# Kernel tuning notes

Hardware: AMD Instinct MI355X
Metric: run time of the kernel (lower is better)

## Reference

```python
import jax, jax.numpy as jnp
import numpy as np

DN = ('NCHW', 'OIHW', 'NCHW')
B, C, H, W = 4, 64, 256, 256
MIP = 8          # max(8, C // 32)
RED = C // 16    # CBAM reduced channels
PS = 8           # FSAS patch size


def conv2d(x, w, padding=0, groups=1):
    return jax.lax.conv_general_dilated(
        x, w, (1, 1), [(padding, padding), (padding, padding)],
        dimension_numbers=DN, feature_group_count=groups)


def bn_eval(x, g, b, eps=1e-5):
    # BatchNorm with init running stats (mean=0, var=1), eval mode
    return x / jnp.sqrt(1.0 + eps) * g[None, :, None, None] + b[None, :, None, None]


def h_swish(x):
    return x * jnp.clip(x + 3.0, 0.0, 6.0) / 6.0


def setup_inputs() -> dict:
    key = jax.random.key(0)
    ks = jax.random.split(key, 12)
    s = 0.05
    d = {
        'x': jax.random.normal(ks[0], (B, C, H, W), jnp.float32),
        # CoordAttention
        'ca_conv1_w': jax.random.normal(ks[1], (MIP, C, 1, 1), jnp.float32) * s,
        'ca_conv1_b': jnp.zeros((MIP,), jnp.float32),
        'ca_bn_g': jnp.ones((MIP,), jnp.float32),
        'ca_bn_b': jnp.zeros((MIP,), jnp.float32),
        'ca_convh_w': jax.random.normal(ks[2], (C, MIP, 1, 1), jnp.float32) * s,
        'ca_convh_b': jnp.zeros((C,), jnp.float32),
        'ca_convw_w': jax.random.normal(ks[3], (C, MIP, 1, 1), jnp.float32) * s,
        'ca_convw_b': jnp.zeros((C,), jnp.float32),
        # FSAS (bias=False)
        'fsas_hidden_w': jax.random.normal(ks[4], (6 * C, C, 1, 1), jnp.float32) * s,
        'fsas_dw_w': jax.random.normal(ks[5], (6 * C, 1, 3, 3), jnp.float32) * s,
        'fsas_proj_w': jax.random.normal(ks[6], (C, 2 * C, 1, 1), jnp.float32) * s,
        'ln_w': jnp.ones((2 * C,), jnp.float32),
        'ln_b': jnp.zeros((2 * C,), jnp.float32),
        # Fusion
        'fus_conv1_w': jax.random.normal(ks[7], (2 * C, 2 * C, 3, 3), jnp.float32) * s,
        'fus_bn1_g': jnp.ones((2 * C,), jnp.float32),
        'fus_bn1_b': jnp.zeros((2 * C,), jnp.float32),
        'fus_conv2_w': jax.random.normal(ks[8], (C, 2 * C, 1, 1), jnp.float32) * s,
        'fus_bn2_g': jnp.ones((C,), jnp.float32),
        'fus_bn2_b': jnp.zeros((C,), jnp.float32),
        # CBAM
        'cbam_mlp1_w': jax.random.normal(ks[9], (RED, C, 1, 1), jnp.float32) * s,
        'cbam_mlp2_w': jax.random.normal(ks[10], (C, RED, 1, 1), jnp.float32) * s,
        'cbam_sa_w': jax.random.normal(ks[11], (1, 2, 7, 7), jnp.float32) * s,
        'residual_scale': jnp.float32(0.1),
    }
    return d


def _forward(x, ca_conv1_w, ca_conv1_b, ca_bn_g, ca_bn_b, ca_convh_w, ca_convh_b,
             ca_convw_w, ca_convw_b, fsas_hidden_w, fsas_dw_w, fsas_proj_w, ln_w, ln_b,
             fus_conv1_w, fus_bn1_g, fus_bn1_b, fus_conv2_w, fus_bn2_g, fus_bn2_b,
             cbam_mlp1_w, cbam_mlp2_w, cbam_sa_w, residual_scale):
    b, c, h, w = x.shape
    c2 = 2 * c

    # ---- CoordAttention branch ----
    xh = jnp.mean(x, axis=3, keepdims=True)                       # [B,C,H,1]
    xw = jnp.mean(x, axis=2, keepdims=True).transpose(0, 1, 3, 2)  # [B,C,W,1]
    y = jnp.concatenate([xh, xw], axis=2)                          # [B,C,H+W,1]
    y = conv2d(y, ca_conv1_w) + ca_conv1_b[None, :, None, None]
    y = h_swish(bn_eval(y, ca_bn_g, ca_bn_b))
    yh, yw = y[:, :, :h], y[:, :, h:]
    yw = yw.transpose(0, 1, 3, 2)
    a_h = jax.nn.sigmoid(conv2d(yh, ca_convh_w) + ca_convh_b[None, :, None, None])
    a_w = jax.nn.sigmoid(conv2d(yw, ca_convw_w) + ca_convw_b[None, :, None, None])
    ca_out = x * a_h * a_w

    # ---- FSAS branch ----
    hid = conv2d(x, fsas_hidden_w)                                 # [B,6C,H,W]
    hid = conv2d(hid, fsas_dw_w, padding=1, groups=6 * c)          # depthwise 3x3
    q, k, v = jnp.split(hid, 3, axis=1)                            # each [B,2C,H,W]

    def patch(t):  # [B,2C,H,W] -> [B,2C,H/8,W/8,8,8]
        return t.reshape(b, c2, h // PS, PS, w // PS, PS).transpose(0, 1, 2, 4, 3, 5)

    qf = jnp.fft.rfft2(patch(q))
    kf = jnp.fft.rfft2(patch(k))
    o = jnp.fft.irfft2(qf * kf, s=(PS, PS))
    o = o.transpose(0, 1, 2, 4, 3, 5).reshape(b, c2, h, w)

    # WithBias LayerNorm over channel dim (per pixel)
    mu = jnp.mean(o, axis=1, keepdims=True)
    var = jnp.var(o, axis=1, keepdims=True)
    on = (o - mu) / jnp.sqrt(var + 1e-5) * ln_w[None, :, None, None] + ln_b[None, :, None, None]
    fsas_out = conv2d(v * on, fsas_proj_w)                         # [B,C,H,W]

    # ---- Fusion ----
    f = conv2d(jnp.concatenate([ca_out, fsas_out], axis=1), fus_conv1_w, padding=1)
    f = jax.nn.gelu(bn_eval(f, fus_bn1_g, fus_bn1_b), approximate=False)
    f = bn_eval(conv2d(f, fus_conv2_w), fus_bn2_g, fus_bn2_b)

    z = x + residual_scale * f

    # ---- CBAM ----
    avg = jnp.mean(z, axis=(2, 3), keepdims=True)
    mx = jnp.max(z, axis=(2, 3), keepdims=True)

    def mlp(t):
        return conv2d(jax.nn.relu(conv2d(t, cbam_mlp1_w)), cbam_mlp2_w)

    z = z * jax.nn.sigmoid(mlp(avg) + mlp(mx))
    sa = jnp.concatenate([jnp.mean(z, axis=1, keepdims=True),
                          jnp.max(z, axis=1, keepdims=True)], axis=1)
    z = z * jax.nn.sigmoid(conv2d(sa, cbam_sa_w, padding=3))
    return jax.nn.gelu(z, approximate=False)


def reference(x, ca_conv1_w, ca_conv1_b, ca_bn_g, ca_bn_b, ca_convh_w, ca_convh_b,
              ca_convw_w, ca_convw_b, fsas_hidden_w, fsas_dw_w, fsas_proj_w, ln_w, ln_b,
              fus_conv1_w, fus_bn1_g, fus_bn1_b, fus_conv2_w, fus_bn2_g, fus_bn2_b,
              cbam_mlp1_w, cbam_mlp2_w, cbam_sa_w, residual_scale):
    return _forward(x, ca_conv1_w, ca_conv1_b, ca_bn_g, ca_bn_b, ca_convh_w, ca_convh_b,
                    ca_convw_w, ca_convw_b, fsas_hidden_w, fsas_dw_w, fsas_proj_w, ln_w, ln_b,
                    fus_conv1_w, fus_bn1_g, fus_bn1_b, fus_conv2_w, fus_bn2_g, fus_bn2_b,
                    cbam_mlp1_w, cbam_mlp2_w, cbam_sa_w, residual_scale)
```

## Files before the change

kernel.cpp:

```cpp
#include <hip/hip_runtime.h>
#include <math.h>

#define B_ 4
#define C_ 64
#define C2_ 128
#define C6_ 384
#define H_ 256
#define Wd_ 256
#define HW_ 65536
#define MIP_ 8
#define BNINV 0.9999950000374994f

typedef short bf16x8 __attribute__((ext_vector_type(8)));
typedef float f32x4 __attribute__((ext_vector_type(4)));
typedef unsigned short u16x8 __attribute__((ext_vector_type(8)));
typedef unsigned short u16x4 __attribute__((ext_vector_type(4)));
typedef unsigned int   u32x4 __attribute__((ext_vector_type(4)));

__device__ __forceinline__ float sigm(float x){ return 1.f/(1.f+expf(-x)); }
__device__ __forceinline__ float gelu_f(float x){ return 0.5f*x*(1.f+erff(x*0.7071067811865476f)); }
__device__ __forceinline__ unsigned short bfrnd(float f){
  unsigned u = __float_as_uint(f);
  unsigned r = u + 0x7FFFu + ((u>>16)&1u);
  return (unsigned short)(r>>16);
}
__device__ __forceinline__ float bf2f(unsigned short s){
  return __uint_as_float(((unsigned)s)<<16);
}

__global__ void k_rowmean(const float* __restrict__ x, float* __restrict__ xh){
  int row = blockIdx.x*4 + (threadIdx.x>>6);
  int lane = threadIdx.x & 63;
  const float* p = x + (size_t)row*Wd_;
  float s = p[lane]+p[lane+64]+p[lane+128]+p[lane+192];
  #pragma unroll
  for(int off=32; off>0; off>>=1) s += __shfl_down(s, off, 64);
  if(lane==0) xh[row] = s*(1.f/Wd_);
}

__global__ void k_colmean(const float* __restrict__ x, float* __restrict__ xw){
  int idx = blockIdx.x*256 + threadIdx.x;
  int w = idx & 255; int bc = idx >> 8;
  const float* p = x + (size_t)bc*HW_ + w;
  float s = 0.f;
  for(int h=0;h<H_;h++) s += p[h*Wd_];
  xw[idx] = s*(1.f/H_);
}

__global__ void k_ca_t(const float* __restrict__ xh, const float* __restrict__ xw,
                       const float* __restrict__ w1, const float* __restrict__ b1,
                       const float* __restrict__ bng, const float* __restrict__ bnb,
                       float* __restrict__ t){
  int idx = blockIdx.x*256 + threadIdx.x;
  int p = idx & 511; int m = (idx>>9)&7; int b = idx>>12;
  float acc = b1[m];
  #pragma unroll 8
  for(int c=0;c<C_;c++){
    float yv = (p<256) ? xh[(b*C_+c)*256 + p] : xw[(b*C_+c)*256 + (p-256)];
    acc += w1[m*C_+c]*yv;
  }
  float v = acc*BNINV*bng[m] + bnb[m];
  t[idx] = v * fminf(fmaxf(v+3.f,0.f),6.f)*(1.f/6.f);
}

__global__ void k_ca_a(const float* __restrict__ t,
                       const float* __restrict__ wh, const float* __restrict__ bh,
                       const float* __restrict__ ww, const float* __restrict__ bw,
                       float* __restrict__ ah, float* __restrict__ aw){
  int idx = blockIdx.x*256 + threadIdx.x;
  int p = idx & 511; int co = (idx>>9)&63; int b = idx>>15;
  bool isH = (p<256);
  const float* wm = isH ? wh : ww;
  float acc = isH ? bh[co] : bw[co];
  #pragma unroll
  for(int m=0;m<MIP_;m++) acc += wm[co*MIP_+m]*t[(b*MIP_+m)*512+p];
  float s = sigm(acc);
  if(isH) ah[(b*C_+co)*256+p] = s; else aw[(b*C_+co)*256+(p-256)] = s;
}

__global__ void __launch_bounds__(256) k_xprep(const float* __restrict__ x, unsigned short* __restrict__ xb){
  __shared__ float sm[64][65];
  int tid = threadIdx.x;
  int img = blockIdx.x >> 10;
  int p0 = (blockIdx.x & 1023)*64;
  int lane = tid & 63, wq = tid >> 6;
  #pragma unroll
  for(int cc=0; cc<16; ++cc){
    int c = cc*4 + wq;
    sm[c][lane] = x[(size_t)(img*C_+c)*HW_ + p0 + lane];
  }
  __syncthreads();
  int pl = tid >> 2;
  int c0 = (tid & 3) * 16;
  u16x8 lo, hi;
  #pragma unroll
  for(int i=0;i<8;i++)  lo[i] = bfrnd(sm[c0+i][pl]);
  #pragma unroll
  for(int i=0;i<8;i++)  hi[i] = bfrnd(sm[c0+8+i][pl]);
  unsigned short* dst = xb + ((size_t)img*HW_ + p0 + pl)*64 + c0;
  *(u16x8*)(dst)     = lo;
  *(u16x8*)(dst + 8) = hi;
}

__global__ void k_wprep(const float* __restrict__ w, unsigned short* __restrict__ wbt){
  int t = blockIdx.x*256 + threadIdx.x;
  const float* src = w + (size_t)t*9;
  int oc = t >> 7, ic = t & 127;
  #pragma unroll
  for(int tap=0; tap<9; ++tap)
    wbt[(size_t)(tap*128+oc)*128 + ic] = bfrnd(src[tap]);
}

__global__ void k_wprep2(const float* __restrict__ pw, const float* __restrict__ w2,
                         const float* __restrict__ hw, unsigned short* __restrict__ pwb,
                         unsigned short* __restrict__ w2b, unsigned short* __restrict__ wb1){
  int t = blockIdx.x*256 + threadIdx.x;
  if(t < 8192){ pwb[t] = bfrnd(pw[t]); w2b[t] = bfrnd(w2[t]); }
  wb1[t] = bfrnd(hw[t]);
}

__global__ void __launch_bounds__(256) k_hid0_mfma(const unsigned short* __restrict__ xb,
                                                   const unsigned short* __restrict__ wb1,
                                                   unsigned short* __restrict__ hid0b){
  int tid = threadIdx.x;
  int lane = tid & 63, wid = tid >> 6;
  int l15 = lane & 15, lk = lane >> 4;
  int p0 = blockIdx.x*128 + wid*32;
  int oc0 = blockIdx.y*96;
  f32x4 acc[6][2];
  #pragma unroll
  for(int m=0;m<6;m++)
    #pragma unroll
    for(int n=0;n<2;n++) acc[m][n] = (f32x4)0.f;
  #pragma unroll
  for(int kk=0; kk<2; ++kk){
    bf16x8 bfr[2];
    #pragma unroll
    for(int n=0;n<2;n++)
      bfr[n] = *(const bf16x8*)(xb + (size_t)(p0 + n*16 + l15)*64 + kk*32 + lk*8);
    #pragma unroll
    for(int m=0;m<6;m++){
      bf16x8 af = *(const bf16x8*)(wb1 + (size_t)(oc0 + m*16 + l15)*64 + kk*32 + lk*8);
      #pragma unroll
      for(int n=0;n<2;n++)
        acc[m][n] = __builtin_amdgcn_mfma_f32_16x16x32_bf16(af, bfr[n], acc[m][n], 0,0,0);
    }
  }
  #pragma unroll
  for(int n=0;n<2;n++){
    int p = p0 + n*16 + l15;
    #pragma unroll
    for(int m=0;m<6;m++){
      u16x4 v;
      #pragma unroll
      for(int r=0;r<4;r++) v[r] = bfrnd(acc[m][n][r]);
      *(u16x4*)(hid0b + (size_t)p*384 + oc0 + m*16 + lk*4) = v;
    }
  }
}

__global__ void __launch_bounds__(256) k_dw_bf(const unsigned short* __restrict__ hid0b,
                                               const float* __restrict__ wd,
                                               unsigned short* __restrict__ hidb){
  int tid = threadIdx.x;
  int cg = tid & 15;
  int tg = tid >> 4;
  int p0 = blockIdx.x*64;
  int h  = p0 >> 8;
  int w0 = (p0 & 255) + tg*4;
  int chb = blockIdx.y*128 + cg*8;

  float wreg[72];
  {
    const f32x4* wsrc = (const f32x4*)(wd + (size_t)chb*9);
    #pragma unroll
    for(int i=0;i<18;i++){
      f32x4 v = wsrc[i];
      wreg[4*i+0]=v[0]; wreg[4*i+1]=v[1]; wreg[4*i+2]=v[2]; wreg[4*i+3]=v[3];
    }
  }
  float acc[4][8];
  #pragma unroll
  for(int px=0;px<4;px++)
    #pragma unroll
    for(int e=0;e<8;e++) acc[px][e] = 0.f;

  #pragma unroll
  for(int ky=0; ky<3; ++ky){
    int hh = h + ky - 1;
    if((unsigned)hh >= 256u) continue;
    float row[6][8];
    #pragma unroll
    for(int c6=0; c6<6; ++c6){
      int ww = w0 + c6 - 1;
      u16x8 v8 = {0,0,0,0,0,0,0,0};
      if((unsigned)ww < 256u)
        v8 = *(const u16x8*)(hid0b + (size_t)(hh*256+ww)*384 + chb);
      #pragma unroll
      for(int e=0;e<8;e++) row[c6][e] = bf2f(v8[e]);
    }
    #pragma unroll
    for(int kx=0; kx<3; ++kx){
      #pragma unroll
      for(int px=0; px<4; ++px){
        #pragma unroll
        for(int e=0;e<8;e++)
          acc[px][e] += row[px+kx][e] * wreg[e*9 + ky*3 + kx];
      }
    }
  }
  #pragma unroll
  for(int px=0; px<4; ++px){
    u16x8 o8;
    #pragma unroll
    for(int e=0;e<8;e++) o8[e] = bfrnd(acc[px][e]);
    *(u16x8*)(hidb + (size_t)(p0 + tg*4 + px)*384 + chb) = o8;
  }
}

__global__ void __launch_bounds__(256) k_circ_bf(const unsigned short* __restrict__ hidb,
                                                 unsigned short* __restrict__ ob){
  __shared__ __align__(16) unsigned short lq[2][64][128];
  __shared__ __align__(16) unsigned short lkk[2][64][128];
  int tid = threadIdx.x;
  #pragma unroll
  for(int it=0; it<8; ++it){
    int s = it*256 + tid;
    int which = s >> 10, rem = s & 1023;
    int pix = rem >> 4, cg = rem & 15;
    int gp = blockIdx.x*2 + which;
    int ph = gp >> 5, pw = gp & 31;
    size_t pg = (size_t)((ph*8 + (pix>>3))*256 + pw*8 + (pix&7));
    *(u16x8*)&lq[which][pix][cg*8]  = *(const u16x8*)(hidb + pg*384 + cg*8);
    *(u16x8*)&lkk[which][pix][cg*8] = *(const u16x8*)(hidb + pg*384 + 128 + cg*8);
  }
  __syncthreads();
  int which = tid >> 7, c = tid & 127;
  float kr[64];
  #pragma unroll
  for(int pix=0;pix<64;pix++) kr[pix] = bf2f(lkk[which][pix][c]);
  float outv[64];
  #pragma unroll
  for(int t2=0;t2<64;t2++) outv[t2] = 0.f;
  #pragma unroll
  for(int u=0;u<8;u++){
    #pragma unroll
    for(int v=0;v<8;v++){
      float qv = bf2f(lq[which][u*8+v][c]);
      #pragma unroll
      for(int i=0;i<8;i++){
        #pragma unroll
        for(int j=0;j<8;j++)
          outv[i*8+j] += qv * kr[((i-u)&7)*8 + ((j-v)&7)];
      }
    }
  }
  __syncthreads();
  #pragma unroll
  for(int t2=0;t2<64;t2++) lq[which][t2][c] = bfrnd(outv[t2]);
  __syncthreads();
  #pragma unroll
  for(int it=0; it<8; ++it){
    int s = it*256 + tid;
    int which2 = s >> 10, rem = s & 1023;
    int pix = rem >> 4, cg = rem & 15;
    int gp = blockIdx.x*2 + which2;
    int ph = gp >> 5, pw = gp & 31;
    size_t pg = (size_t)((ph*8 + (pix>>3))*256 + pw*8 + (pix&7));
    *(u16x8*)(ob + pg*128 + cg*8) = *(u16x8*)&lq[which2][pix][cg*8];
  }
}

__global__ void __launch_bounds__(256) k_proj_mfma(const unsigned short* __restrict__ ob,
                      const unsigned short* __restrict__ hidb,
                      const float* __restrict__ lnw, const float* __restrict__ lnb,
                      const unsigned short* __restrict__ pwb, unsigned short* __restrict__ catb){
  __shared__ unsigned int lds32[256*64];
  int tid = threadIdx.x;
  int lane = tid & 63, wid = tid >> 6;
  int p0 = blockIdx.x*256;
  {
    int p = p0 + tid;
    u16x8 o8[16];
    #pragma unroll
    for(int g=0; g<16; ++g) o8[g] = *(const u16x8*)(ob + (size_t)p*128 + g*8);
    float s=0.f, s2=0.f;
    #pragma unroll
    for(int g=0; g<16; ++g)
      #pragma unroll
      for(int e=0; e<8; ++e){ float v = bf2f(o8[g][e]); s += v; s2 += v*v; }
    float m = s*(1.f/C2_);
    float var = s2*(1.f/C2_) - m*m;
    float rs = rsqrtf(var + 1e-5f);
    #pragma unroll
    for(int cg=0; cg<16; ++cg){
      u16x8 v8 = *(const u16x8*)(hidb + (size_t)p*384 + 256 + cg*8);
      unsigned uu[4];
      #pragma unroll
      for(int ee=0; ee<4; ++ee){
        int c = cg*8 + ee*2;
        float on0 = (bf2f(o8[cg][2*ee])   - m)*rs*lnw[c]   + lnb[c];
        float on1 = (bf2f(o8[cg][2*ee+1]) - m)*rs*lnw[c+1] + lnb[c+1];
        float vn0 = bf2f(v8[2*ee])*on0;
        float vn1 = bf2f(v8[2*ee+1])*on1;
        uu[ee] = (unsigned)bfrnd(vn0) | ((unsigned)bfrnd(vn1)<<16);
      }
      int blk = cg ^ (tid & 15);
      u32x4 w4 = {uu[0],uu[1],uu[2],uu[3]};
      *(u32x4*)&lds32[tid*64 + blk*4] = w4;
    }
  }
  __syncthreads();
  int l15 = lane & 15, lk = lane >> 4;
  f32x4 acc[4][4];
  #pragma unroll
  for(int m=0;m<4;m++)
    #pragma unroll
    for(int n=0;n<4;n++) acc[m][n] = (f32x4)0.f;
  int plb = wid*64;
  #pragma unroll
  for(int kk=0; kk<4; ++kk){
    bf16x8 bfr[4];
    #pragma unroll
    for(int n=0;n<4;n++){
      int pl = plb + n*16 + l15;
      int blk = (kk*4 + lk) ^ l15;
      bfr[n] = *(bf16x8*)&lds32[pl*64 + blk*4];
    }
    #pragma unroll
    for(int m=0;m<4;m++){
      bf16x8 af = *(const bf16x8*)(pwb + (size_t)(m*16+l15)*128 + kk*32 + lk*8);
      #pragma unroll
      for(int n=0;n<4;n++)
        acc[m][n] = __builtin_amdgcn_mfma_f32_16x16x32_bf16(af, bfr[n], acc[m][n], 0,0,0);
    }
  }
  #pragma unroll
  for(int n=0;n<4;n++){
    int p = p0 + plb + n*16 + l15;
    #pragma unroll
    for(int m=0;m<4;m++){
      u16x4 v;
      #pragma unroll
      for(int r=0;r<4;r++) v[r] = bfrnd(acc[m][n][r]);
      *(u16x4*)(catb + (size_t)p*128 + 64 + m*16 + lk*4) = v;
    }
  }
}

__global__ void __launch_bounds__(256) k_caout_bf(const float* __restrict__ x, const float* __restrict__ ah,
                        const float* __restrict__ aw, unsigned short* __restrict__ catb, int b){
  __shared__ float sm[64][65];
  int tid = threadIdx.x;
  int p0 = blockIdx.x*64;
  int h = p0 >> 8;
  int wbase = p0 & 255;
  int lane = tid & 63, wq = tid >> 6;
  #pragma unroll
  for(int cc=0; cc<16; ++cc){
    int c = cc*4 + wq;
    float v = x[(size_t)(b*C_+c)*HW_ + p0 + lane];
    v *= ah[(b*C_+c)*256 + h] * aw[(b*C_+c)*256 + wbase + lane];
    sm[c][lane] = v;
  }
  __syncthreads();
  int pl = tid >> 2;
  int c0 = (tid & 3) * 16;
  u16x8 lo, hi;
  #pragma unroll
  for(int i=0;i<8;i++)  lo[i] = bfrnd(sm[c0+i][pl]);
  #pragma unroll
  for(int i=0;i<8;i++)  hi[i] = bfrnd(sm[c0+8+i][pl]);
  unsigned short* dst = catb + (size_t)(p0+pl)*128 + c0;
  *(u16x8*)(dst)     = lo;
  *(u16x8*)(dst + 8) = hi;
}

__global__ void __launch_bounds__(256,3) k_fus1_mfma(const unsigned short* __restrict__ catb,
                                                     const unsigned short* __restrict__ wbt,
                                                     unsigned short* __restrict__ f1b){
  __shared__ __align__(16) unsigned short sA[3][130][32];
  int tid = threadIdx.x;
  int lane = tid & 63, wid = tid >> 6;
  int wm = wid & 1, wn = wid >> 1;
  int bid = blockIdx.x;
  int xcd = bid & 7, idx = bid >> 3;
  int h   = xcd*32 + (idx >> 2);
  int w0  = ((idx >> 1) & 1) * 128;
  int ocb = (idx & 1) * 64 + wn*32;
  int l15 = lane & 15, lk = lane >> 4;

  f32x4 acc[4][2];
  #pragma unroll
  for(int i=0;i<4;i++)
    #pragma unroll
    for(int j=0;j<2;j++) acc[i][j] = (f32x4)0.f;

  const unsigned short* wbase = wbt + (size_t)(ocb + l15)*128 + lk*8;

  for(int icc=0; icc<4; ++icc){
    int ic0 = icc*32;
    __syncthreads();
    #pragma unroll
    for(int it=0; it<7; ++it){
      int s = it*256 + tid;
      if(s < 1560){
        int row = s/520;
        int rem = s - row*520;
        int pxl = rem >> 2;
        int icq = rem & 3;
        int r = h + row - 1;
        int c = w0 + pxl - 1;
        u16x8 v = {0,0,0,0,0,0,0,0};
        if((unsigned)r < 256u && (unsigned)c < 256u)
          v = *(const u16x8*)(catb + (size_t)(r*256 + c)*128 + ic0 + icq*8);
        int blk = icq ^ ((pxl>>1)&3);
        *(u16x8*)&sA[row][pxl][blk*8] = v;
      }
    }
    __syncthreads();
    bf16x8 wf[9][2];
    #pragma unroll
    for(int tap=0; tap<9; ++tap){
      const unsigned short* wt = wbase + (size_t)tap*16384 + ic0;
      wf[tap][0] = *(const bf16x8*)(wt);
      wf[tap][1] = *(const bf16x8*)(wt + 2048);
    }
    #pragma unroll
    for(int ky=0; ky<3; ++ky){
      #pragma unroll
      for(int kx=0; kx<3; ++kx){
        #pragma unroll
        for(int i=0;i<4;++i){
          int rr = wm*64 + i*16 + l15 + kx;
          int blk = lk ^ ((rr>>1)&3);
          bf16x8 a = *(const bf16x8*)&sA[ky][rr][blk*8];
          acc[i][0] = __builtin_amdgcn_mfma_f32_16x16x32_bf16(wf[ky*3+kx][0], a, acc[i][0], 0,0,0);
          acc[i][1] = __builtin_amdgcn_mfma_f32_16x16x32_bf16(wf[ky*3+kx][1], a, acc[i][1], 0,0,0);
        }
      }
    }
  }
  #pragma unroll
  for(int i=0;i<4;i++){
    int sp = h*256 + w0 + wm*64 + i*16 + l15;
    #pragma unroll
    for(int j=0;j<2;j++){
      u16x4 v;
      #pragma unroll
      for(int r2=0;r2<4;r2++) v[r2] = bfrnd(acc[i][j][r2]);
      *(u16x4*)(f1b + (size_t)sp*128 + ocb + j*16 + lk*4) = v;
    }
  }
}

__global__ void __launch_bounds__(256) k_fus2_mfma(const unsigned short* __restrict__ f1b,
                      const float* __restrict__ x, const unsigned short* __restrict__ w2b,
                      const float* __restrict__ bn1g, const float* __restrict__ bn1b,
                      const float* __restrict__ bn2g, const float* __restrict__ bn2b,
                      const float* __restrict__ rscale, float* __restrict__ z,
                      float* __restrict__ psum2, float* __restrict__ pmax2, int b){
  __shared__ unsigned int lds32[128*64];
  __shared__ float smp[4][4][16], smm[4][4][16];
  int tid = threadIdx.x;
  int lane = tid & 63, wid = tid >> 6;
  int p0 = blockIdx.x*128;
  int ic0 = (tid & 15) * 8;
  #pragma unroll
  for(int pass=0; pass<8; ++pass){
    int pl = pass*16 + (tid>>4);
    bf16x8 vv = *(const bf16x8*)(f1b + (size_t)(p0+pl)*128 + ic0);
    unsigned uu[4];
    #pragma unroll
    for(int ee=0; ee<4; ++ee){
      float f0 = bf2f((unsigned short)vv[2*ee])  *BNINV*bn1g[ic0+2*ee]   + bn1b[ic0+2*ee];
      float f1 = bf2f((unsigned short)vv[2*ee+1])*BNINV*bn1g[ic0+2*ee+1] + bn1b[ic0+2*ee+1];
      uu[ee] = (unsigned)bfrnd(gelu_f(f0)) | ((unsigned)bfrnd(gelu_f(f1))<<16);
    }
    int blk = (ic0>>3) ^ (pl&15);
    u32x4 w4 = {uu[0],uu[1],uu[2],uu[3]};
    *(u32x4*)&lds32[pl*64 + blk*4] = w4;
  }
  __syncthreads();
  int l15 = lane & 15, lk = lane >> 4;
  f32x4 acc[4][2];
  #pragma unroll
  for(int m=0;m<4;m++)
    #pragma unroll
    for(int n=0;n<2;n++) acc[m][n] = (f32x4)0.f;
  int pl0 = wid*32 + l15;
  #pragma unroll
  for(int kk=0; kk<4; ++kk){
    bf16x8 bfr[2];
    #pragma unroll
    for(int n=0;n<2;n++){
      int pl = pl0 + n*16;
      int blk = (kk*4 + lk) ^ l15;
      bfr[n] = *(bf16x8*)&lds32[pl*64 + blk*4];
    }
    #pragma unroll
    for(int m=0;m<4;m++){
      bf16x8 af = *(const bf16x8*)(w2b + (size_t)(m*16+l15)*128 + kk*32 + lk*8);
      #pragma unroll
      for(int n=0;n<2;n++)
        acc[m][n] = __builtin_amdgcn_mfma_f32_16x16x32_bf16(af, bfr[n], acc[m][n], 0,0,0);
    }
  }
  float rs = rscale[0];
  float ps[4][4], pm[4][4];
  #pragma unroll
  for(int m=0;m<4;m++)
    #pragma unroll
    for(int r=0;r<4;r++){ ps[m][r]=0.f; pm[m][r]=-INFINITY; }
  #pragma unroll
  for(int n=0;n<2;n++){
    int p = p0 + pl0 + n*16;
    #pragma unroll
    for(int m=0;m<4;m++){
      #pragma unroll
      for(int r=0;r<4;r++){
        int oc = m*16 + lk*4 + r;
        float f = acc[m][n][r]*BNINV*bn2g[oc] + bn2b[oc];
        float zv = x[(size_t)(b*C_+oc)*HW_ + p] + rs*f;
        z[(size_t)oc*HW_ + p] = zv;
        ps[m][r] += zv; pm[m][r] = fmaxf(pm[m][r], zv);
      }
    }
  }
  #pragma unroll
  for(int off=1; off<16; off<<=1){
    #pragma unroll
    for(int m=0;m<4;m++)
      #pragma unroll
      for(int r=0;r<4;r++){
        ps[m][r] += __shfl_xor(ps[m][r], off, 64);
        pm[m][r] = fmaxf(pm[m][r], __shfl_xor(pm[m][r], off, 64));
      }
  }
  if(l15 == 0){
    #pragma unroll
    for(int m=0;m<4;m++)
      #pragma unroll
      for(int r=0;r<4;r++){
        smp[wid][lk][m*4+r] = ps[m][r];
        smm[wid][lk][m*4+r] = pm[m][r];
      }
  }
  __syncthreads();
  if(tid < 64){
    int m = tid>>4, lkg = (tid>>2)&3, r = tid&3;
    float s = 0.f, mx = -INFINITY;
    #pragma unroll
    for(int w=0;w<4;w++){
      s += smp[w][lkg][m*4+r];
      mx = fmaxf(mx, smm[w][lkg][m*4+r]);
    }
    psum2[blockIdx.x*64 + tid] = s;
    pmax2[blockIdx.x*64 + tid] = mx;
  }
}

__global__ void k_cbamred2(const float* __restrict__ psum2, const float* __restrict__ pmax2,
                           float* __restrict__ avgb, float* __restrict__ maxb){
  int c = blockIdx.x; int tid = threadIdx.x;
  float s = psum2[(size_t)tid*64 + c] + psum2[(size_t)(tid+256)*64 + c];
  float m = fmaxf(pmax2[(size_t)tid*64 + c], pmax2[(size_t)(tid+256)*64 + c]);
  __shared__ float ss[256], sm[256];
  ss[tid]=s; sm[tid]=m; __syncthreads();
  for(int off=128; off>0; off>>=1){
    if(tid<off){ ss[tid]+=ss[tid+off]; sm[tid]=fmaxf(sm[tid],sm[tid+off]); }
    __syncthreads();
  }
  if(tid==0){ avgb[c]=ss[0]*(1.f/HW_); maxb[c]=sm[0]; }
}

__global__ void k_cbammlp(const float* __restrict__ avgb, const float* __restrict__ maxb,
                          const float* __restrict__ w1, const float* __restrict__ w2,
                          float* __restrict__ catt){
  __shared__ float h1s[8];
  int tid = threadIdx.x;
  if(tid<8){
    const float* src = (tid<4)? avgb : maxb;
    int r = tid & 3;
    float s = 0.f;
    for(int c=0;c<C_;c++) s += w1[r*C_+c]*src[c];
    h1s[tid] = fmaxf(s,0.f);
  }
  __syncthreads();
  float a = 0.f;
  #pragma unroll
  for(int r=0;r<4;r++) a += w2[tid*4+r]*(h1s[r]+h1s[r+4]);
  catt[tid] = sigm(a);
}

__global__ void k_chatt(const float* __restrict__ z, const float* __restrict__ catt,
                        float* __restrict__ samean, float* __restrict__ samax){
  int p = blockIdx.x*256 + threadIdx.x;
  float s = 0.f, m = -INFINITY;
  #pragma unroll 8
  for(int c=0;c<C_;c++){
    float v = z[(size_t)c*HW_+p]*catt[c];
    s += v; m = fmaxf(m,v);
  }
  samean[p] = s*(1.f/C_);
  samax[p] = m;
}

__global__ void k_saconv(const float* __restrict__ samean, const float* __restrict__ samax,
                         const float* __restrict__ saw, float* __restrict__ att){
  int p = blockIdx.x*256 + threadIdx.x;
  int h = p>>8, w = p&255;
  float acc = 0.f;
  #pragma unroll
  for(int ky=0;ky<7;ky++){
    int hh = h+ky-3; if((unsigned)hh>=256u) continue;
    #pragma unroll
    for(int kx=0;kx<7;kx++){
      int ww2 = w+kx-3; if((unsigned)ww2>=256u) continue;
      int q = hh*256+ww2;
      acc += samean[q]*saw[ky*7+kx] + samax[q]*saw[49+ky*7+kx];
    }
  }
  att[p] = sigm(acc);
}

__global__ void k_final(const float* __restrict__ z, const float* __restrict__ catt,
                        const float* __restrict__ att, float* __restrict__ out, int b){
  int p = blockIdx.x*256 + threadIdx.x;
  int c = blockIdx.y;
  float v = z[(size_t)c*HW_+p]*catt[c]*att[p];
  out[(size_t)(b*C_+c)*HW_+p] = gelu_f(v);
}

extern "C" void kernel_launch(void* const* d_in, const int* in_sizes, int n_in,
                              void* d_out, int out_size, void* d_ws, size_t ws_size,
                              hipStream_t stream){
  const float* x            = (const float*)d_in[0];
  const float* ca_conv1_w   = (const float*)d_in[1];
  const float* ca_conv1_b   = (const float*)d_in[2];
  const float* ca_bn_g      = (const float*)d_in[3];
  const float* ca_bn_b      = (const float*)d_in[4];
  const float* ca_convh_w   = (const float*)d_in[5];
  const float* ca_convh_b   = (const float*)d_in[6];
  const float* ca_convw_w   = (const float*)d_in[7];
  const float* ca_convw_b   = (const float*)d_in[8];
  const float* fsas_hidden_w= (const float*)d_in[9];
  const float* fsas_dw_w    = (const float*)d_in[10];
  const float* fsas_proj_w  = (const float*)d_in[11];
  const float* ln_w         = (const float*)d_in[12];
  const float* ln_b         = (const float*)d_in[13];
  const float* fus_conv1_w  = (const float*)d_in[14];
  const float* fus_bn1_g    = (const float*)d_in[15];
  const float* fus_bn1_b    = (const float*)d_in[16];
  const float* fus_conv2_w  = (const float*)d_in[17];
  const float* fus_bn2_g    = (const float*)d_in[18];
  const float* fus_bn2_b    = (const float*)d_in[19];
  const float* cbam_mlp1_w  = (const float*)d_in[20];
  const float* cbam_mlp2_w  = (const float*)d_in[21];
  const float* cbam_sa_w    = (const float*)d_in[22];
  const float* rscale       = (const float*)d_in[23];
  float* out = (float*)d_out;
  float* ws  = (float*)d_ws;

  float* xh     = ws + 0;
  float* xw     = ws + 65536;
  float* t      = ws + 131072;
  float* ah     = ws + 147456;
  float* aw     = ws + 212992;
  float* catt   = ws + 278528;
  float* avgb   = ws + 278592;
  float* maxb   = ws + 278656;
  float* psum2  = ws + 278720;
  float* pmax2  = ws + 311488;
  float* samean = ws + 344256;
  float* samax  = ws + 409792;
  float* att    = ws + 475328;
  float* big    = ws + 540864;
  unsigned short* catb  = (unsigned short*)(big);
  unsigned short* f1b   = (unsigned short*)(big + 4194304);
  float*          z     =                  big + 8388608;
  unsigned short* xb    = (unsigned short*)(big + 12582912);
  unsigned short* hid0b = (unsigned short*)(big + 20971520);
  unsigned short* hidb  = (unsigned short*)(big + 33554432);
  unsigned short* obuf  = (unsigned short*)(big + 46137344);
  unsigned short* wbt   = (unsigned short*)(big + 50331648);
  unsigned short* wb1   = (unsigned short*)(big + 50405376);
  unsigned short* pwb   = (unsigned short*)(big + 50417664);
  unsigned short* w2b   = (unsigned short*)(big + 50421760);

  k_rowmean<<<16384,256,0,stream>>>(x, xh);
  k_colmean<<<256,256,0,stream>>>(x, xw);
  k_ca_t<<<64,256,0,stream>>>(xh, xw, ca_conv1_w, ca_conv1_b, ca_bn_g, ca_bn_b, t);
  k_ca_a<<<512,256,0,stream>>>(t, ca_convh_w, ca_convh_b, ca_convw_w, ca_convw_b, ah, aw);
  k_xprep<<<4096,256,0,stream>>>(x, xb);
  k_wprep<<<64,256,0,stream>>>(fus_conv1_w, wbt);
  k_wprep2<<<96,256,0,stream>>>(fsas_proj_w, fus_conv2_w, fsas_hidden_w, pwb, w2b, wb1);

  for(int b=0;b<4;b++){
    k_hid0_mfma<<<dim3(512,4),256,0,stream>>>(xb + (size_t)b*HW_*64, wb1, hid0b);
    k_dw_bf<<<dim3(1024,3),256,0,stream>>>(hid0b, fsas_dw_w, hidb);
    k_circ_bf<<<512,256,0,stream>>>(hidb, obuf);
    k_proj_mfma<<<256,256,0,stream>>>(obuf, hidb, ln_w, ln_b, pwb, catb);
    k_caout_bf<<<1024,256,0,stream>>>(x, ah, aw, catb, b);
    k_fus1_mfma<<<1024,256,0,stream>>>(catb, wbt, f1b);
    k_fus2_mfma<<<512,256,0,stream>>>(f1b, x, w2b, fus_bn1_g, fus_bn1_b, fus_bn2_g, fus_bn2_b,
                                      rscale, z, psum2, pmax2, b);
    k_cbamred2<<<64,256,0,stream>>>(psum2, pmax2, avgb, maxb);
    k_cbammlp<<<1,64,0,stream>>>(avgb, maxb, cbam_mlp1_w, cbam_mlp2_w, catt);
    k_chatt<<<256,256,0,stream>>>(z, catt, samean, samax);
    k_saconv<<<256,256,0,stream>>>(samean, samax, cbam_sa_w, att);
    k_final<<<dim3(256,64),256,0,stream>>>(z, catt, att, out, b);
  }
}
```

Measured before the change: 839.1 us.

## Register-prefetch next input-channel slice in fus1 conv while computing current

The fus1 3x3 conv kernel now loads the next 32-channel slice of the input tile from global memory into registers right after the shared-memory store barrier, so the load latency overlaps the MFMA work on the current slice. Tile index math is precomputed once per thread. Weight fragments are now loaded per kernel row (3 taps) instead of all 9 at once, which reduces register pressure. Holding 7 u16x8 staging registers across the compute loop costs VGPRs and may lower occupancy under launch_bounds(256,3).

```diff
diff --git a/kernel.cpp b/kernel.cpp
--- a/kernel.cpp
+++ b/kernel.cpp
@@ -390,6 +390,33 @@
   int ocb = (idx & 1) * 64 + wn*32;
   int l15 = lane & 15, lk = lane >> 4;
 
+  int srow[7], spxl[7], sicq[7];
+  bool sok[7], sld[7];
+  #pragma unroll
+  for(int it=0; it<7; ++it){
+    int s = it*256 + tid;
+    sok[it] = (s < 1560);
+    int row = s/520;
+    int rem = s - row*520;
+    int pxl = rem >> 2;
+    int icq = rem & 3;
+    srow[it]=row; spxl[it]=pxl; sicq[it]=icq;
+    int r = h + row - 1;
+    int c = w0 + pxl - 1;
+    sld[it] = sok[it] && (unsigned)r < 256u && (unsigned)c < 256u;
+  }
+
+  u16x8 st[7];
+  #pragma unroll
+  for(int it=0; it<7; ++it){
+    u16x8 v = {0,0,0,0,0,0,0,0};
+    if(sld[it]){
+      int r = h + srow[it] - 1, c = w0 + spxl[it] - 1;
+      v = *(const u16x8*)(catb + (size_t)(r*256 + c)*128 + sicq[it]*8);
+    }
+    st[it] = v;
+  }
+
   f32x4 acc[4][2];
   #pragma unroll
   for(int i=0;i<4;i++)
@@ -403,31 +430,33 @@
     __syncthreads();
     #pragma unroll
     for(int it=0; it<7; ++it){
-      int s = it*256 + tid;
-      if(s < 1560){
-        int row = s/520;
-        int rem = s - row*520;
-        int pxl = rem >> 2;
-        int icq = rem & 3;
-        int r = h + row - 1;
-        int c = w0 + pxl - 1;
+      if(sok[it]){
+        int blk = sicq[it] ^ ((spxl[it]>>1)&3);
+        *(u16x8*)&sA[srow[it]][spxl[it]][blk*8] = st[it];
+      }
+    }
+    __syncthreads();
+    if(icc < 3){
+      int ic0n = (icc+1)*32;
+      #pragma unroll
+      for(int it=0; it<7; ++it){
         u16x8 v = {0,0,0,0,0,0,0,0};
-        if((unsigned)r < 256u && (unsigned)c < 256u)
-          v = *(const u16x8*)(catb + (size_t)(r*256 + c)*128 + ic0 + icq*8);
-        int blk = icq ^ ((pxl>>1)&3);
-        *(u16x8*)&sA[row][pxl][blk*8] = v;
-      }
-    }
-    __syncthreads();
-    bf16x8 wf[9][2];
-    #pragma unroll
-    for(int tap=0; tap<9; ++tap){
-      const unsigned short* wt = wbase + (size_t)tap*16384 + ic0;
-      wf[tap][0] = *(const bf16x8*)(wt);
-      wf[tap][1] = *(const bf16x8*)(wt + 2048);
+        if(sld[it]){
+          int r = h + srow[it] - 1, c = w0 + spxl[it] - 1;
+          v = *(const u16x8*)(catb + (size_t)(r*256 + c)*128 + ic0n + sicq[it]*8);
+        }
+        st[it] = v;
+      }
     }
     #pragma unroll
     for(int ky=0; ky<3; ++ky){
+      bf16x8 wf[3][2];
+      #pragma unroll
+      for(int kx=0; kx<3; ++kx){
+        const unsigned short* wt = wbase + (size_t)(ky*3+kx)*16384 + ic0;
+        wf[kx][0] = *(const bf16x8*)(wt);
+        wf[kx][1] = *(const bf16x8*)(wt + 2048);
+      }
       #pragma unroll
       for(int kx=0; kx<3; ++kx){
         #pragma unroll
@@ -435,8 +464,8 @@
           int rr = wm*64 + i*16 + l15 + kx;
           int blk = lk ^ ((rr>>1)&3);
           bf16x8 a = *(const bf16x8*)&sA[ky][rr][blk*8];
-          acc[i][0] = __builtin_amdgcn_mfma_f32_16x16x32_bf16(wf[ky*3+kx][0], a, acc[i][0], 0,0,0);
-          acc[i][1] = __builtin_amdgcn_mfma_f32_16x16x32_bf16(wf[ky*3+kx][1], a, acc[i][1], 0,0,0);
+          acc[i][0] = __builtin_amdgcn_mfma_f32_16x16x32_bf16(wf[kx][0], a, acc[i][0], 0,0,0);
+          acc[i][1] = __builtin_amdgcn_mfma_f32_16x16x32_bf16(wf[kx][1], a, acc[i][1], 0,0,0);
         }
       }
     }
```

New measurement: 824.9 us. About the same (-1.7%).
